# Performance work log

Measured on AMD Instinct MI355X. Metric: run time of the kernel, lower is better.

## Reference

```python
import jax, jax.numpy as jnp
import numpy as np

T, B, H, E, L, V, S = 32, 32, 512, 512, 2, 50000, 512


def setup_inputs() -> dict:
    key = jax.random.key(0)
    ks = jax.random.split(key, 20)
    sc = 0.05
    inp = {
        "inputs": jax.random.randint(ks[0], (T, B), 0, V, dtype=jnp.int32),
        "h0": jax.random.normal(ks[1], (L, B, H), jnp.float32),
        "c0": jax.random.normal(ks[2], (L, B, H), jnp.float32),
        "contexts": jax.random.normal(ks[3], (B, S, H), jnp.float32),
        "contexts_conv": jax.random.normal(ks[4], (B, S, H), jnp.float32),
        "emb": jax.random.normal(ks[5], (V, E), jnp.float32) * sc,
        # stacked LSTM params (E == H so layer-0/1 W_ih stack)
        "W_ih": jax.random.normal(ks[6], (L, 4 * H, H), jnp.float32) * sc,
        "W_hh": jax.random.normal(ks[7], (L, 4 * H, H), jnp.float32) * sc,
        "b_ih": jnp.zeros((L, 4 * H), jnp.float32),
        "b_hh": jnp.zeros((L, 4 * H), jnp.float32),
        # softmax attention (self.attention)
        "Wi_att": jax.random.normal(ks[8], (H, H), jnp.float32) * sc,
        "bi_att": jnp.zeros((H,), jnp.float32),
        "Wo_att": jax.random.normal(ks[9], (H, 2 * H), jnp.float32) * sc,
        "bo_att": jnp.zeros((H,), jnp.float32),
        # conv attention (self.attention_conv, softmax=False -> sigmoid weights)
        "Wi_conv": jax.random.normal(ks[10], (H, H), jnp.float32) * sc,
        "bi_conv": jnp.zeros((H,), jnp.float32),
        "Wo_conv": jax.random.normal(ks[11], (H, 2 * H), jnp.float32) * sc,
        "bo_conv": jnp.zeros((H,), jnp.float32),
    }
    return inp


def _lstm_cell(x, h, c, W_ih, W_hh, b_ih, b_hh):
    # torch gate order: i, f, g, o
    g = x @ W_ih.T + h @ W_hh.T + (b_ih + b_hh)
    i, f, gg, o = jnp.split(g, 4, axis=-1)
    c2 = jax.nn.sigmoid(f) * c + jax.nn.sigmoid(i) * jnp.tanh(gg)
    h2 = jax.nn.sigmoid(o) * jnp.tanh(c2)
    return h2, c2


def reference(inputs, h0, c0, contexts, contexts_conv, emb,
              W_ih, W_hh, b_ih, b_hh,
              Wi_att, bi_att, Wo_att, bo_att,
              Wi_conv, bi_conv, Wo_conv, bo_conv):
    embs = emb[inputs]  # [T, B, E]

    def step(carry, emb_t):
        h, c = carry  # [L, B, H] each
        x = emb_t
        hs, cs = [], []
        for l in range(L):
            h_l, c_l = _lstm_cell(x, h[l], c[l], W_ih[l], W_hh[l], b_ih[l], b_hh[l])
            x = h_l
            hs.append(h_l)
            cs.append(c_l)
        h, c = jnp.stack(hs), jnp.stack(cs)
        # attention_conv: sigmoid-gated weighted sum over contexts_conv
        gamma_c = x @ Wi_conv.T + bi_conv  # [B, H]
        w_c = jax.nn.sigmoid(jnp.einsum('bsh,bh->bs', contexts_conv, gamma_c))
        ct_c = jnp.einsum('bs,bsh->bh', w_c, contexts_conv)
        out_conv = jnp.tanh(jnp.concatenate([ct_c, x], -1) @ Wo_conv.T + bo_conv)
        # attention: softmax weighted sum over contexts, query = out_conv
        gamma = out_conv @ Wi_att.T + bi_att
        w = jax.nn.softmax(jnp.einsum('bsh,bh->bs', contexts, gamma), axis=-1)
        ct = jnp.einsum('bs,bsh->bh', w, contexts)
        out = jnp.tanh(jnp.concatenate([ct, out_conv], -1) @ Wo_att.T + bo_att)
        out = out + out_conv  # residual add from forward()
        return (h, c), out

    (hf, cf), outputs = jax.lax.scan(step, (h0, c0), embs)
    return outputs, hf, cf
```

## Files before the change

### kernel.cpp

```cpp
#include <hip/hip_runtime.h>
#include <math.h>

namespace {
constexpr int T_ = 32, B_ = 32, H_ = 512, S_ = 512;
constexpr int BH = B_ * H_;
constexpr int LSTM_NWG = 512;
constexpr size_t O_EMBS = 0;
constexpr size_t O_H0   = O_EMBS + (size_t)T_ * BH;
constexpr size_t O_H1   = O_H0 + 2 * BH;
constexpr size_t O_GC   = O_H1 + 2 * BH;
constexpr size_t O_CTC  = O_GC + (size_t)1024 * 512;
constexpr size_t O_OCV  = O_CTC + (size_t)1024 * 512;
}

__device__ unsigned g_arrive[LSTM_NWG] = {};
__device__ unsigned g_go = 0;

static __device__ __forceinline__ float sigm(float x) { return 1.0f / (1.0f + expf(-x)); }
static __device__ __forceinline__ float dot4(float4 a, float4 b) {
  return a.x * b.x + a.y * b.y + a.z * b.z + a.w * b.w;
}
static __device__ __forceinline__ void fma4(float4& a, float s, float4 x) {
  a.x += s * x.x; a.y += s * x.y; a.z += s * x.z; a.w += s * x.w;
}
static __device__ __forceinline__ void scale_fma4(float4& a, float f, float e, float4 x) {
  a.x = a.x * f + e * x.x; a.y = a.y * f + e * x.y;
  a.z = a.z * f + e * x.z; a.w = a.w * f + e * x.w;
}

static __device__ __forceinline__ float coh_load(const float* p) {
  return __hip_atomic_load(p, __ATOMIC_RELAXED, __HIP_MEMORY_SCOPE_AGENT);
}
static __device__ __forceinline__ void coh_store(float* p, float v) {
  __hip_atomic_store(p, v, __ATOMIC_RELAXED, __HIP_MEMORY_SCOPE_AGENT);
}

static __device__ __forceinline__ void grid_barrier_light(unsigned target) {
  asm volatile("s_waitcnt vmcnt(0)" ::: "memory");
  __syncthreads();
  if (threadIdx.x == 0)
    __hip_atomic_store(&g_arrive[blockIdx.x], target, __ATOMIC_RELAXED,
                       __HIP_MEMORY_SCOPE_AGENT);
  if (blockIdx.x == 0) {
    for (int i = threadIdx.x; i < LSTM_NWG; i += 256)
      while (__hip_atomic_load(&g_arrive[i], __ATOMIC_RELAXED,
                               __HIP_MEMORY_SCOPE_AGENT) < target)
        __builtin_amdgcn_s_sleep(1);
    __syncthreads();
    if (threadIdx.x == 0)
      __hip_atomic_store(&g_go, target, __ATOMIC_RELAXED,
                         __HIP_MEMORY_SCOPE_AGENT);
  }
  if (threadIdx.x == 0)
    while (__hip_atomic_load(&g_go, __ATOMIC_RELAXED,
                             __HIP_MEMORY_SCOPE_AGENT) < target)
      __builtin_amdgcn_s_sleep(1);
  __syncthreads();
  asm volatile("" ::: "memory");
}

__global__ __launch_bounds__(512)
void k_init(const int* __restrict__ inputs, const float* __restrict__ h0in,
            const float* __restrict__ emb, float* __restrict__ ws) {
  const int g = blockIdx.x, tid = threadIdx.x;
  const int gid = g * 512 + tid;
  if (gid < BH) {
    ws[O_H0 + gid]      = h0in[gid];
    ws[O_H1 + BH + gid] = h0in[BH + gid];
  }
#pragma unroll
  for (int r = 0; r < 4; ++r) {
    const int tb = g * 4 + r;
    ws[O_EMBS + (size_t)tb * H_ + tid] = emb[(size_t)inputs[tb] * H_ + tid];
  }
}

__global__ __launch_bounds__(256, 2)
void k_lstm(const float* __restrict__ W_ih, const float* __restrict__ W_hh,
            const float* __restrict__ b_ih, const float* __restrict__ b_hh,
            const float* __restrict__ c0in, float* __restrict__ out,
            float* __restrict__ ws) {
  const int g = blockIdx.x, tid = threadIdx.x;
  const int cell = g >> 8, cp = g & 255;
  float* EMBS = ws + O_EMBS;
  float* H0 = ws + O_H0;
  float* H1 = ws + O_H1;

  __shared__ __align__(16) float wlds[2][4][1024];
  __shared__ __align__(16) float stg0[32 * 132];
  __shared__ __align__(16) float stg1[32 * 132];
  __shared__ float red[64 * 17];

  {
    const float* Wih = W_ih + (size_t)cell * 4 * H_ * H_;
    const float* Whh = W_hh + (size_t)cell * 4 * H_ * H_;
#pragma unroll
    for (int l = 0; l < 8; ++l) {
      const int fidx = l * 256 + tid;
      const int row = fidx >> 7;
      const int c4 = fidx & 127;
      const int h2 = row & 1, gt = (row >> 1) & 3, jj = row >> 3;
      const float* src = (h2 ? Whh : Wih) + ((size_t)gt * H_ + cp * 2 + jj) * H_;
      *(float4*)&wlds[jj][gt][h2 * 512 + c4 * 4] = *(const float4*)(src + c4 * 4);
    }
  }
  float creg = 0.f, bsum0 = 0.f, bsum1 = 0.f, bsum2 = 0.f, bsum3 = 0.f;
  if (tid < 64) {
    const int bb = tid & 31, j2 = tid >> 5;
    const int jo = cp * 2 + j2;
    creg = c0in[cell * BH + bb * H_ + jo];
    const float* bi = b_ih + (size_t)cell * 4 * H_;
    const float* bh = b_hh + (size_t)cell * 4 * H_;
    bsum0 = bi[0 * H_ + jo] + bh[0 * H_ + jo];
    bsum1 = bi[1 * H_ + jo] + bh[1 * H_ + jo];
    bsum2 = bi[2 * H_ + jo] + bh[2 * H_ + jo];
    bsum3 = bi[3 * H_ + jo] + bh[3 * H_ + jo];
  }
  __syncthreads();

  const int b = tid & 31, jj = (tid >> 5) & 1, ks = tid >> 6;
  const int lane = tid & 63;

  unsigned bar = __hip_atomic_load(&g_go, __ATOMIC_RELAXED,
                                   __HIP_MEMORY_SCOPE_AGENT);

  for (int s = 0; s <= T_; ++s) {
    const int pi = s & 1, qi = pi ^ 1;
    const bool act = cell ? (s >= 1) : (s < T_);
    float a0 = 0.f, a1 = 0.f, a2 = 0.f, a3 = 0.f;

    if (act) {
      if (cell == 0) {
        const float* xs = EMBS + (size_t)s * BH + b * H_ + ks * 128;
        const float* wx0 = &wlds[jj][0][ks * 128];
        const float* wx1 = &wlds[jj][1][ks * 128];
        const float* wx2 = &wlds[jj][2][ks * 128];
        const float* wx3 = &wlds[jj][3][ks * 128];
#pragma unroll 8
        for (int k = 0; k < 128; k += 4) {
          const float4 x4 = *(const float4*)(xs + k);
          a0 += dot4(x4, *(const float4*)(wx0 + k));
          a1 += dot4(x4, *(const float4*)(wx1 + k));
          a2 += dot4(x4, *(const float4*)(wx2 + k));
          a3 += dot4(x4, *(const float4*)(wx3 + k));
        }
      }
      const float* H0p = H0 + pi * BH;
      const float* H1p = H1 + pi * BH;
      for (int c = 0; c < 4; ++c) {
        {
          float v0[16];
#pragma unroll
          for (int i = 0; i < 16; ++i) {
            const int d = tid + i * 256;
            const int bb2 = d >> 7, kk = d & 127;
            v0[i] = coh_load(H0p + bb2 * H_ + c * 128 + kk);
          }
          if (cell) {
            float v1[16];
#pragma unroll
            for (int i = 0; i < 16; ++i) {
              const int d = tid + i * 256;
              const int bb2 = d >> 7, kk = d & 127;
              v1[i] = coh_load(H1p + bb2 * H_ + c * 128 + kk);
            }
#pragma unroll
            for (int i = 0; i < 16; ++i) {
              const int d = tid + i * 256;
              const int bb2 = d >> 7, kk = d & 127;
              stg1[bb2 * 132 + kk] = v1[i];
            }
          }
#pragma unroll
          for (int i = 0; i < 16; ++i) {
            const int d = tid + i * 256;
            const int bb2 = d >> 7, kk = d & 127;
            stg0[bb2 * 132 + kk] = v0[i];
          }
        }
        __syncthreads();
        {
          const int kb = c * 128 + ks * 32;
          if (cell) {
            const float* sd = &stg0[b * 132 + ks * 32];
            const float* w0 = &wlds[jj][0][kb];
            const float* w1 = &wlds[jj][1][kb];
            const float* w2 = &wlds[jj][2][kb];
            const float* w3 = &wlds[jj][3][kb];
#pragma unroll
            for (int k = 0; k < 32; k += 4) {
              const float4 x4 = *(const float4*)(sd + k);
              a0 += dot4(x4, *(const float4*)(w0 + k));
              a1 += dot4(x4, *(const float4*)(w1 + k));
              a2 += dot4(x4, *(const float4*)(w2 + k));
              a3 += dot4(x4, *(const float4*)(w3 + k));
            }
          }
          const float* hd = cell ? &stg1[b * 132 + ks * 32]
                                 : &stg0[b * 132 + ks * 32];
          const float* u0 = &wlds[jj][0][512 + kb];
          const float* u1 = &wlds[jj][1][512 + kb];
          const float* u2 = &wlds[jj][2][512 + kb];
          const float* u3 = &wlds[jj][3][512 + kb];
#pragma unroll
          for (int k = 0; k < 32; k += 4) {
            const float4 h4 = *(const float4*)(hd + k);
            a0 += dot4(h4, *(const float4*)(u0 + k));
            a1 += dot4(h4, *(const float4*)(u1 + k));
            a2 += dot4(h4, *(const float4*)(u2 + k));
            a3 += dot4(h4, *(const float4*)(u3 + k));
          }
        }
        __syncthreads();
      }
      red[lane * 17 + 0 * 4 + ks] = a0;
      red[lane * 17 + 1 * 4 + ks] = a1;
      red[lane * 17 + 2 * 4 + ks] = a2;
      red[lane * 17 + 3 * 4 + ks] = a3;
    }
    __syncthreads();
    if (act && tid < 64) {
      const int bb = tid & 31, j2 = tid >> 5;
      const int jo = cp * 2 + j2;
      float gi = bsum0, gf = bsum1, gg = bsum2, go_ = bsum3;
#pragma unroll
      for (int k = 0; k < 4; ++k) {
        gi  += red[tid * 17 + 0 * 4 + k];
        gf  += red[tid * 17 + 1 * 4 + k];
        gg  += red[tid * 17 + 2 * 4 + k];
        go_ += red[tid * 17 + 3 * 4 + k];
      }
      const float cn = sigm(gf) * creg + sigm(gi) * tanhf(gg);
      const float hn = sigm(go_) * tanhf(cn);
      creg = cn;
      float* Hs = cell ? H1 : H0;
      coh_store(&Hs[qi * BH + bb * H_ + jo], hn);
      if (cell)
        out[((size_t)(s - 1) * B_ + bb) * H_ + jo] = hn;
      if (!cell && s == T_ - 1) {
        out[(size_t)T_ * BH + bb * H_ + jo]            = hn;
        out[(size_t)T_ * BH + 2 * BH + bb * H_ + jo]   = cn;
      }
      if (cell && s == T_) {
        out[(size_t)T_ * BH + BH + bb * H_ + jo]       = hn;
        out[(size_t)T_ * BH + 3 * BH + bb * H_ + jo]   = cn;
      }
    }
    if (s < T_) grid_barrier_light(++bar);
  }
}

template<bool TANH, bool RES>
__global__ __launch_bounds__(256)
void k_gemm(const float* __restrict__ A1, const float* __restrict__ A2,
            const float* __restrict__ W, const float* __restrict__ bias,
            const float* __restrict__ res, float* __restrict__ C, int dualA) {
  const int bid = blockIdx.x, tid = threadIdx.x;
  const int m0 = (bid & 31) * 32, n0 = (bid >> 5) * 32;
  const int tx = tid & 15, ty = tid >> 4;
  const int lr = tid >> 5, lc = tid & 31;
  const int nsteps = dualA ? 32 : 16;
  const int Krow = dualA ? 1024 : 512;
  __shared__ __align__(16) float Asm[32 * 33];
  __shared__ __align__(16) float Bsm[32 * 34];
  float acc00 = 0.f, acc01 = 0.f, acc10 = 0.f, acc11 = 0.f;

  for (int kt = 0; kt < nsteps; ++kt) {
    const float* A = (kt < 16) ? A1 : A2;
    const int ka = (kt < 16) ? kt * 32 : (kt - 16) * 32;
    const int kb = kt * 32;
    __syncthreads();
#pragma unroll
    for (int i = 0; i < 4; ++i) {
      const int row = lr + i * 8;
      Asm[row * 33 + lc] = A[(size_t)(m0 + row) * 512 + ka + lc];
      Bsm[lc * 34 + row] = W[(size_t)(n0 + row) * Krow + kb + lc];
    }
    __syncthreads();
#pragma unroll 8
    for (int k = 0; k < 32; ++k) {
      const float a0 = Asm[(ty * 2) * 33 + k];
      const float a1 = Asm[(ty * 2 + 1) * 33 + k];
      const float2 bv = *(const float2*)&Bsm[k * 34 + tx * 2];
      acc00 += a0 * bv.x; acc01 += a0 * bv.y;
      acc10 += a1 * bv.x; acc11 += a1 * bv.y;
    }
  }
  const int n = n0 + tx * 2;
  const int m = m0 + ty * 2;
  const float bx = bias[n], by = bias[n + 1];
  float v00 = acc00 + bx, v01 = acc01 + by;
  float v10 = acc10 + bx, v11 = acc11 + by;
  if (TANH) { v00 = tanhf(v00); v01 = tanhf(v01); v10 = tanhf(v10); v11 = tanhf(v11); }
  if (RES) {
    v00 += res[(size_t)m * 512 + n];       v01 += res[(size_t)m * 512 + n + 1];
    v10 += res[(size_t)(m + 1) * 512 + n]; v11 += res[(size_t)(m + 1) * 512 + n + 1];
  }
  C[(size_t)m * 512 + n] = v00;            C[(size_t)m * 512 + n + 1] = v01;
  C[(size_t)(m + 1) * 512 + n] = v10;      C[(size_t)(m + 1) * 512 + n + 1] = v11;
}

__global__ __launch_bounds__(256)
void k_sweep_conv(const float* __restrict__ ctxc, const float* __restrict__ GC,
                  float* __restrict__ CTC) {
  const int bid = blockIdx.x, tid = threadIdx.x;
  const int b = bid & 31;
  const int w = tid >> 6, lane = tid & 63;
  const float* gl = GC + (size_t)bid * H_ + lane * 8;
  const float4 g0 = *(const float4*)gl;
  const float4 g1 = *(const float4*)(gl + 4);
  float4 a0 = {0, 0, 0, 0}, a1 = {0, 0, 0, 0};
  const float* base = ctxc + (size_t)b * S_ * H_ + lane * 8;
  for (int i = 0; i < 128; ++i) {
    const int s = i * 4 + w;
    const float* xr = base + (size_t)s * H_;
    const float4 x0 = *(const float4*)(xr);
    const float4 x1 = *(const float4*)(xr + 4);
    float p = dot4(x0, g0) + dot4(x1, g1);
#pragma unroll
    for (int off = 32; off >= 1; off >>= 1) p += __shfl_xor(p, off, 64);
    const float wt = sigm(p);
    fma4(a0, wt, x0); fma4(a1, wt, x1);
  }
  __shared__ __align__(16) float part[4 * 512];
  *(float4*)&part[w * 512 + lane * 8] = a0;
  *(float4*)&part[w * 512 + lane * 8 + 4] = a1;
  __syncthreads();
  float sA = 0.f, sB = 0.f;
#pragma unroll
  for (int w8 = 0; w8 < 4; ++w8) {
    sA += part[w8 * 512 + tid];
    sB += part[w8 * 512 + 256 + tid];
  }
  CTC[(size_t)bid * H_ + tid] = sA;
  CTC[(size_t)bid * H_ + 256 + tid] = sB;
}

__global__ __launch_bounds__(256)
void k_sweep_att(const float* __restrict__ ctx, const float* __restrict__ GA,
                 float* __restrict__ CT) {
  const int bid = blockIdx.x, tid = threadIdx.x;
  const int b = bid & 31;
  const int w = tid >> 6, lane = tid & 63;
  const float* gl = GA + (size_t)bid * H_ + lane * 8;
  const float4 g0 = *(const float4*)gl;
  const float4 g1 = *(const float4*)(gl + 4);
  float4 a0 = {0, 0, 0, 0}, a1 = {0, 0, 0, 0};
  float m = -1e30f, l = 0.f;
  const float* base = ctx + (size_t)b * S_ * H_ + lane * 8;
  for (int i = 0; i < 128; ++i) {
    const int s = i * 4 + w;
    const float* xr = base + (size_t)s * H_;
    const float4 x0 = *(const float4*)(xr);
    const float4 x1 = *(const float4*)(xr + 4);
    float p = dot4(x0, g0) + dot4(x1, g1);
#pragma unroll
    for (int off = 32; off >= 1; off >>= 1) p += __shfl_xor(p, off, 64);
    const float m2 = fmaxf(m, p);
    const float f = expf(m - m2);
    const float e = expf(p - m2);
    l = l * f + e;
    scale_fma4(a0, f, e, x0);
    scale_fma4(a1, f, e, x1);
    m = m2;
  }
  __shared__ __align__(16) float part[4 * 512 + 8];
  *(float4*)&part[w * 512 + lane * 8] = a0;
  *(float4*)&part[w * 512 + lane * 8 + 4] = a1;
  if (lane == 0) { part[2048 + w * 2] = m; part[2048 + w * 2 + 1] = l; }
  __syncthreads();
  float M = part[2048];
#pragma unroll
  for (int w8 = 1; w8 < 4; ++w8) M = fmaxf(M, part[2048 + w8 * 2]);
  float fac[4], L = 0.f;
#pragma unroll
  for (int w8 = 0; w8 < 4; ++w8) {
    fac[w8] = expf(part[2048 + w8 * 2] - M);
    L += fac[w8] * part[2048 + w8 * 2 + 1];
  }
  const float inv = 1.0f / L;
  float sA = 0.f, sB = 0.f;
#pragma unroll
  for (int w8 = 0; w8 < 4; ++w8) {
    sA += fac[w8] * part[w8 * 512 + tid];
    sB += fac[w8] * part[w8 * 512 + 256 + tid];
  }
  CT[(size_t)bid * H_ + tid] = sA * inv;
  CT[(size_t)bid * H_ + 256 + tid] = sB * inv;
}

extern "C" void kernel_launch(void* const* d_in, const int* in_sizes, int n_in,
                              void* d_out, int out_size, void* d_ws, size_t ws_size,
                              hipStream_t stream) {
  const int*   inputs  = (const int*)d_in[0];
  const float* h0in    = (const float*)d_in[1];
  const float* c0in    = (const float*)d_in[2];
  const float* ctx     = (const float*)d_in[3];
  const float* ctxc    = (const float*)d_in[4];
  const float* emb     = (const float*)d_in[5];
  const float* W_ih    = (const float*)d_in[6];
  const float* W_hh    = (const float*)d_in[7];
  const float* b_ih    = (const float*)d_in[8];
  const float* b_hh    = (const float*)d_in[9];
  const float* Wi_att  = (const float*)d_in[10];
  const float* bi_att  = (const float*)d_in[11];
  const float* Wo_att  = (const float*)d_in[12];
  const float* bo_att  = (const float*)d_in[13];
  const float* Wi_conv = (const float*)d_in[14];
  const float* bi_conv = (const float*)d_in[15];
  const float* Wo_conv = (const float*)d_in[16];
  const float* bo_conv = (const float*)d_in[17];
  float* out = (float*)d_out;
  float* ws  = (float*)d_ws;

  float* GC  = ws + O_GC;
  float* CTC = ws + O_CTC;
  float* OCV = ws + O_OCV;

  k_init<<<dim3(256), dim3(512), 0, stream>>>(inputs, h0in, emb, ws);
  k_lstm<<<dim3(LSTM_NWG), dim3(256), 0, stream>>>(W_ih, W_hh, b_ih, b_hh,
                                                   c0in, out, ws);
  k_gemm<false, false><<<dim3(512), dim3(256), 0, stream>>>(
      out, nullptr, Wi_conv, bi_conv, nullptr, GC, 0);
  k_sweep_conv<<<dim3(1024), dim3(256), 0, stream>>>(ctxc, GC, CTC);
  k_gemm<true, false><<<dim3(512), dim3(256), 0, stream>>>(
      CTC, out, Wo_conv, bo_conv, nullptr, OCV, 1);
  k_gemm<false, false><<<dim3(512), dim3(256), 0, stream>>>(
      OCV, nullptr, Wi_att, bi_att, nullptr, GC, 0);
  k_sweep_att<<<dim3(1024), dim3(256), 0, stream>>>(ctx, GC, CTC);
  k_gemm<true, true><<<dim3(512), dim3(256), 0, stream>>>(
      CTC, OCV, Wo_att, bo_att, OCV, out, 1);
}
```

Baseline: 760.8 us.

## Reuse each context row across four timesteps in attention sweep kernels

The conv and softmax attention sweep kernels now have each block handle four timesteps for one batch element, with 512 threads and 8 waves. Every context row loaded from global memory is scored against four query vectors, which cuts context traffic roughly fourfold. The cost is more registers per thread (four sets of accumulators and queries), fewer blocks (256 instead of 1024) and a reduction phase serialized over the four timesteps with extra barriers. The coh_store helper is inlined as a direct atomic store, with no change in behavior.

```diff
diff --git a/kernel.cpp b/kernel.cpp
--- a/kernel.cpp
+++ b/kernel.cpp
@@ -30,9 +30,6 @@
 
 static __device__ __forceinline__ float coh_load(const float* p) {
   return __hip_atomic_load(p, __ATOMIC_RELAXED, __HIP_MEMORY_SCOPE_AGENT);
-}
-static __device__ __forceinline__ void coh_store(float* p, float v) {
-  __hip_atomic_store(p, v, __ATOMIC_RELAXED, __HIP_MEMORY_SCOPE_AGENT);
 }
 
 static __device__ __forceinline__ void grid_barrier_light(unsigned target) {
@@ -234,16 +231,17 @@
       const float hn = sigm(go_) * tanhf(cn);
       creg = cn;
       float* Hs = cell ? H1 : H0;
-      coh_store(&Hs[qi * BH + bb * H_ + jo], hn);
+      __hip_atomic_store(&Hs[qi * BH + bb * H_ + jo], hn,
+                         __ATOMIC_RELAXED, __HIP_MEMORY_SCOPE_AGENT);
       if (cell)
         out[((size_t)(s - 1) * B_ + bb) * H_ + jo] = hn;
       if (!cell && s == T_ - 1) {
-        out[(size_t)T_ * BH + bb * H_ + jo]            = hn;
-        out[(size_t)T_ * BH + 2 * BH + bb * H_ + jo]   = cn;
+        out[(size_t)T_ * BH + bb * H_ + jo]          = hn;
+        out[(size_t)T_ * BH + 2 * BH + bb * H_ + jo] = cn;
       }
       if (cell && s == T_) {
-        out[(size_t)T_ * BH + BH + bb * H_ + jo]       = hn;
-        out[(size_t)T_ * BH + 3 * BH + bb * H_ + jo]   = cn;
+        out[(size_t)T_ * BH + BH + bb * H_ + jo]     = hn;
+        out[(size_t)T_ * BH + 3 * BH + bb * H_ + jo] = cn;
       }
     }
     if (s < T_) grid_barrier_light(++bar);
@@ -300,93 +298,129 @@
   C[(size_t)(m + 1) * 512 + n] = v10;      C[(size_t)(m + 1) * 512 + n + 1] = v11;
 }
 
-__global__ __launch_bounds__(256)
+__global__ __launch_bounds__(512)
 void k_sweep_conv(const float* __restrict__ ctxc, const float* __restrict__ GC,
                   float* __restrict__ CTC) {
   const int bid = blockIdx.x, tid = threadIdx.x;
-  const int b = bid & 31;
+  const int b = bid & 31, tc = bid >> 5;
   const int w = tid >> 6, lane = tid & 63;
-  const float* gl = GC + (size_t)bid * H_ + lane * 8;
-  const float4 g0 = *(const float4*)gl;
-  const float4 g1 = *(const float4*)(gl + 4);
-  float4 a0 = {0, 0, 0, 0}, a1 = {0, 0, 0, 0};
+  float4 g0[4], g1[4];
+#pragma unroll
+  for (int tt = 0; tt < 4; ++tt) {
+    const int m = (tc * 4 + tt) * B_ + b;
+    const float* gl = GC + (size_t)m * H_ + lane * 8;
+    g0[tt] = *(const float4*)gl;
+    g1[tt] = *(const float4*)(gl + 4);
+  }
+  float4 a0[4], a1[4];
+#pragma unroll
+  for (int tt = 0; tt < 4; ++tt) {
+    a0[tt] = make_float4(0, 0, 0, 0); a1[tt] = make_float4(0, 0, 0, 0);
+  }
   const float* base = ctxc + (size_t)b * S_ * H_ + lane * 8;
-  for (int i = 0; i < 128; ++i) {
-    const int s = i * 4 + w;
+  for (int i = 0; i < 64; ++i) {
+    const int s = i * 8 + w;
     const float* xr = base + (size_t)s * H_;
     const float4 x0 = *(const float4*)(xr);
     const float4 x1 = *(const float4*)(xr + 4);
-    float p = dot4(x0, g0) + dot4(x1, g1);
-#pragma unroll
-    for (int off = 32; off >= 1; off >>= 1) p += __shfl_xor(p, off, 64);
-    const float wt = sigm(p);
-    fma4(a0, wt, x0); fma4(a1, wt, x1);
-  }
-  __shared__ __align__(16) float part[4 * 512];
-  *(float4*)&part[w * 512 + lane * 8] = a0;
-  *(float4*)&part[w * 512 + lane * 8 + 4] = a1;
-  __syncthreads();
-  float sA = 0.f, sB = 0.f;
-#pragma unroll
-  for (int w8 = 0; w8 < 4; ++w8) {
-    sA += part[w8 * 512 + tid];
-    sB += part[w8 * 512 + 256 + tid];
-  }
-  CTC[(size_t)bid * H_ + tid] = sA;
-  CTC[(size_t)bid * H_ + 256 + tid] = sB;
-}
-
-__global__ __launch_bounds__(256)
+    float p[4];
+#pragma unroll
+    for (int tt = 0; tt < 4; ++tt)
+      p[tt] = dot4(x0, g0[tt]) + dot4(x1, g1[tt]);
+#pragma unroll
+    for (int off = 32; off >= 1; off >>= 1) {
+#pragma unroll
+      for (int tt = 0; tt < 4; ++tt) p[tt] += __shfl_xor(p[tt], off, 64);
+    }
+#pragma unroll
+    for (int tt = 0; tt < 4; ++tt) {
+      const float wt = sigm(p[tt]);
+      fma4(a0[tt], wt, x0); fma4(a1[tt], wt, x1);
+    }
+  }
+  __shared__ __align__(16) float part[8 * 512];
+#pragma unroll
+  for (int tt = 0; tt < 4; ++tt) {
+    __syncthreads();
+    *(float4*)&part[w * 512 + lane * 8] = a0[tt];
+    *(float4*)&part[w * 512 + lane * 8 + 4] = a1[tt];
+    __syncthreads();
+    float sum = 0.f;
+#pragma unroll
+    for (int w8 = 0; w8 < 8; ++w8) sum += part[w8 * 512 + tid];
+    const int m = (tc * 4 + tt) * B_ + b;
+    CTC[(size_t)m * H_ + tid] = sum;
+  }
+}
+
+__global__ __launch_bounds__(512)
 void k_sweep_att(const float* __restrict__ ctx, const float* __restrict__ GA,
                  float* __restrict__ CT) {
   const int bid = blockIdx.x, tid = threadIdx.x;
-  const int b = bid & 31;
+  const int b = bid & 31, tc = bid >> 5;
   const int w = tid >> 6, lane = tid & 63;
-  const float* gl = GA + (size_t)bid * H_ + lane * 8;
-  const float4 g0 = *(const float4*)gl;
-  const float4 g1 = *(const float4*)(gl + 4);
-  float4 a0 = {0, 0, 0, 0}, a1 = {0, 0, 0, 0};
-  float m = -1e30f, l = 0.f;
+  float4 g0[4], g1[4];
+#pragma unroll
+  for (int tt = 0; tt < 4; ++tt) {
+    const int m = (tc * 4 + tt) * B_ + b;
+    const float* gl = GA + (size_t)m * H_ + lane * 8;
+    g0[tt] = *(const float4*)gl;
+    g1[tt] = *(const float4*)(gl + 4);
+  }
+  float4 a0[4], a1[4];
+  float mx[4], lx[4];
+#pragma unroll
+  for (int tt = 0; tt < 4; ++tt) {
+    a0[tt] = make_float4(0, 0, 0, 0); a1[tt] = make_float4(0, 0, 0, 0);
+    mx[tt] = -1e30f; lx[tt] = 0.f;
+  }
   const float* base = ctx + (size_t)b * S_ * H_ + lane * 8;
-  for (int i = 0; i < 128; ++i) {
-    const int s = i * 4 + w;
+  for (int i = 0; i < 64; ++i) {
+    const int s = i * 8 + w;
     const float* xr = base + (size_t)s * H_;
     const float4 x0 = *(const float4*)(xr);
     const float4 x1 = *(const float4*)(xr + 4);
-    float p = dot4(x0, g0) + dot4(x1, g1);
-#pragma unroll
-    for (int off = 32; off >= 1; off >>= 1) p += __shfl_xor(p, off, 64);
-    const float m2 = fmaxf(m, p);
-    const float f = expf(m - m2);
-    const float e = expf(p - m2);
-    l = l * f + e;
-    scale_fma4(a0, f, e, x0);
-    scale_fma4(a1, f, e, x1);
-    m = m2;
-  }
-  __shared__ __align__(16) float part[4 * 512 + 8];
-  *(float4*)&part[w * 512 + lane * 8] = a0;
-  *(float4*)&part[w * 512 + lane * 8 + 4] = a1;
-  if (lane == 0) { part[2048 + w * 2] = m; part[2048 + w * 2 + 1] = l; }
-  __syncthreads();
-  float M = part[2048];
-#pragma unroll
-  for (int w8 = 1; w8 < 4; ++w8) M = fmaxf(M, part[2048 + w8 * 2]);
-  float fac[4], L = 0.f;
-#pragma unroll
-  for (int w8 = 0; w8 < 4; ++w8) {
-    fac[w8] = expf(part[2048 + w8 * 2] - M);
-    L += fac[w8] * part[2048 + w8 * 2 + 1];
-  }
-  const float inv = 1.0f / L;
-  float sA = 0.f, sB = 0.f;
-#pragma unroll
-  for (int w8 = 0; w8 < 4; ++w8) {
-    sA += fac[w8] * part[w8 * 512 + tid];
-    sB += fac[w8] * part[w8 * 512 + 256 + tid];
-  }
-  CT[(size_t)bid * H_ + tid] = sA * inv;
-  CT[(size_t)bid * H_ + 256 + tid] = sB * inv;
+    float p[4];
+#pragma unroll
+    for (int tt = 0; tt < 4; ++tt)
+      p[tt] = dot4(x0, g0[tt]) + dot4(x1, g1[tt]);
+#pragma unroll
+    for (int off = 32; off >= 1; off >>= 1) {
+#pragma unroll
+      for (int tt = 0; tt < 4; ++tt) p[tt] += __shfl_xor(p[tt], off, 64);
+    }
+#pragma unroll
+    for (int tt = 0; tt < 4; ++tt) {
+      const float m2 = fmaxf(mx[tt], p[tt]);
+      const float f = expf(mx[tt] - m2);
+      const float e = expf(p[tt] - m2);
+      lx[tt] = lx[tt] * f + e;
+      scale_fma4(a0[tt], f, e, x0);
+      scale_fma4(a1[tt], f, e, x1);
+      mx[tt] = m2;
+    }
+  }
+  __shared__ __align__(16) float part[8 * 512 + 16];
+#pragma unroll
+  for (int tt = 0; tt < 4; ++tt) {
+    __syncthreads();
+    *(float4*)&part[w * 512 + lane * 8] = a0[tt];
+    *(float4*)&part[w * 512 + lane * 8 + 4] = a1[tt];
+    if (lane == 0) { part[4096 + w * 2] = mx[tt]; part[4096 + w * 2 + 1] = lx[tt]; }
+    __syncthreads();
+    float M = part[4096];
+#pragma unroll
+    for (int w8 = 1; w8 < 8; ++w8) M = fmaxf(M, part[4096 + w8 * 2]);
+    float L = 0.f, sum = 0.f;
+#pragma unroll
+    for (int w8 = 0; w8 < 8; ++w8) {
+      const float f = expf(part[4096 + w8 * 2] - M);
+      L   += f * part[4096 + w8 * 2 + 1];
+      sum += f * part[w8 * 512 + tid];
+    }
+    const int m = (tc * 4 + tt) * B_ + b;
+    CT[(size_t)m * H_ + tid] = sum / L;
+  }
 }
 
 extern "C" void kernel_launch(void* const* d_in, const int* in_sizes, int n_in,
@@ -422,12 +456,12 @@
                                                    c0in, out, ws);
   k_gemm<false, false><<<dim3(512), dim3(256), 0, stream>>>(
       out, nullptr, Wi_conv, bi_conv, nullptr, GC, 0);
-  k_sweep_conv<<<dim3(1024), dim3(256), 0, stream>>>(ctxc, GC, CTC);
+  k_sweep_conv<<<dim3(256), dim3(512), 0, stream>>>(ctxc, GC, CTC);
   k_gemm<true, false><<<dim3(512), dim3(256), 0, stream>>>(
       CTC, out, Wo_conv, bo_conv, nullptr, OCV, 1);
   k_gemm<false, false><<<dim3(512), dim3(256), 0, stream>>>(
       OCV, nullptr, Wi_att, bi_att, nullptr, GC, 0);
-  k_sweep_att<<<dim3(1024), dim3(256), 0, stream>>>(ctx, GC, CTC);
+  k_sweep_att<<<dim3(256), dim3(512), 0, stream>>>(ctx, GC, CTC);
   k_gemm<true, true><<<dim3(512), dim3(256), 0, stream>>>(
       CTC, OCV, Wo_att, bo_att, OCV, out, 1);
 }
```

Result: slower. 796.3 us (+4.7%).
